# Performance work log

Hardware: AMD Instinct MI355X
Metric: run time of the kernel (lower is better)

Reference implementation:

```python
import jax, jax.numpy as jnp
import numpy as np

N = 50000      # nodes
E = 800000     # edges (before self-loops)
F_IN = 256     # input features
HID = 32       # per-head hidden channels, conv1
H1 = 4         # heads conv1 (concat)
H2 = 4         # heads conv2 (mean)
NCLS = 40      # output classes
NEG_SLOPE = 0.2
SM_EPS = 1e-16  # PyG softmax denominator eps
LN_EPS = 1e-5


def setup_inputs() -> dict:
    key = jax.random.key(0)
    ks = jax.random.split(key, 12)
    s1 = 1.0 / np.sqrt(F_IN)
    s2 = 1.0 / np.sqrt(H1 * HID)
    return {
        "x": jax.random.normal(ks[0], (N, F_IN), dtype=jnp.float32),
        "edge_index": jax.random.randint(ks[1], (2, E), 0, N, dtype=jnp.int32),
        "W1": jax.random.normal(ks[2], (F_IN, H1 * HID), dtype=jnp.float32) * s1,
        "att_src1": jax.random.normal(ks[3], (H1, HID), dtype=jnp.float32) * s1,
        "att_dst1": jax.random.normal(ks[4], (H1, HID), dtype=jnp.float32) * s1,
        "b1": jnp.zeros((H1 * HID,), jnp.float32),
        "W2": jax.random.normal(ks[5], (H1 * HID, H2 * NCLS), dtype=jnp.float32) * s2,
        "att_src2": jax.random.normal(ks[6], (H2, NCLS), dtype=jnp.float32) * s2,
        "att_dst2": jax.random.normal(ks[7], (H2, NCLS), dtype=jnp.float32) * s2,
        "b2": jnp.zeros((NCLS,), jnp.float32),
        "ln0_g": jnp.ones((H1 * HID,), jnp.float32),
        "ln0_b": jnp.zeros((H1 * HID,), jnp.float32),
        "ln1_g": jnp.ones((NCLS,), jnp.float32),
        "ln1_b": jnp.zeros((NCLS,), jnp.float32),
    }


def gat_conv(x, edge_index, W, a_src, a_dst, bias, heads, ch, concat):
    """PyG GATConv: self-loops, edge attention, per-dst segment softmax, scatter-sum."""
    n = x.shape[0]
    loops = jnp.arange(n, dtype=edge_index.dtype)
    src = jnp.concatenate([edge_index[0], loops])  # message source
    dst = jnp.concatenate([edge_index[1], loops])  # aggregation target
    h = (x @ W).reshape(n, heads, ch)              # [N,H,C]
    e_src = jnp.einsum('nhc,hc->nh', h, a_src)     # [N,H]
    e_dst = jnp.einsum('nhc,hc->nh', h, a_dst)
    e = jax.nn.leaky_relu(e_src[src] + e_dst[dst], NEG_SLOPE)  # [E',H]
    m = jax.ops.segment_max(e, dst, num_segments=n)            # stable softmax max
    p = jnp.exp(e - m[dst])
    denom = jax.ops.segment_sum(p, dst, num_segments=n)
    alpha = p / (denom[dst] + SM_EPS)                          # [E',H]
    out = jax.ops.segment_sum(h[src] * alpha[:, :, None], dst, num_segments=n)  # [N,H,C]
    out = out.reshape(n, heads * ch) if concat else out.mean(axis=1)
    return out + bias


def layer_norm(x, g, b):
    mu = x.mean(axis=-1, keepdims=True)
    var = jnp.mean((x - mu) ** 2, axis=-1, keepdims=True)
    return (x - mu) * jax.lax.rsqrt(var + LN_EPS) * g + b


def reference(x, edge_index, W1, att_src1, att_dst1, b1, W2, att_src2, att_dst2, b2,
              ln0_g, ln0_b, ln1_g, ln1_b):
    # eval mode: dropout = identity
    h = gat_conv(x, edge_index, W1, att_src1, att_dst1, b1, H1, HID, True)
    h = layer_norm(jax.nn.elu(h), ln0_g, ln0_b)
    h = gat_conv(h, edge_index, W2, att_src2, att_dst2, b2, H2, NCLS, False)
    h = layer_norm(h, ln1_g, ln1_b)
    return jax.nn.log_softmax(h, axis=1)
```

## Files before the change

### kernel.cpp

```cpp
#include <hip/hip_runtime.h>
#include <hip/hip_bf16.h>
#include <hip/hip_fp16.h>

#define NNODES 50000
#define NEDGES 800000
#define FIN    256
#define HEADS  4
#define C1     32
#define D1     128
#define C2     40
#define D2     160
#define CAP    64

#define RB1 144
#define RB2 88
#define ZB  ((NNODES + 255) / 256)
#define FB  (NEDGES / 256)
#define GB1 ((NNODES + 63) / 64)

typedef unsigned short u16;
typedef short v8s __attribute__((ext_vector_type(8)));
typedef float v4f __attribute__((ext_vector_type(4)));

__device__ __forceinline__ float bf2f(unsigned u) {
    union { unsigned u; float f; } x; x.u = u << 16; return x.f;
}
__device__ __forceinline__ u16 f2bf(float f) {
    unsigned u = __float_as_uint(f);
    return (u16)((u + 0x7fff + ((u >> 16) & 1)) >> 16);
}
__device__ __forceinline__ unsigned pk_bf16(float a, float b) {
    unsigned ua = (__float_as_uint(a) + 0x8000u) >> 16;
    unsigned ub = (__float_as_uint(b) + 0x8000u) & 0xffff0000u;
    return ub | ua;
}
__device__ __forceinline__ float wave_sum(float v) {
    #pragma unroll
    for (int m = 32; m > 0; m >>= 1) v += __shfl_xor(v, m, 64);
    return v;
}
__device__ __forceinline__ void wave_sum2(float& a, float& b) {
    #pragma unroll
    for (int m = 32; m > 0; m >>= 1) {
        a += __shfl_xor(a, m, 64);
        b += __shfl_xor(b, m, 64);
    }
}
__device__ __forceinline__ float leaky(float x) { return fmaxf(x, 0.2f * x); }

__device__ __forceinline__ void repack_body(const float* __restrict__ W,
                                            const float* __restrict__ as,
                                            const float* __restrict__ ad,
                                            u16* __restrict__ Wf,
                                            int K, int N, int C, int total, int idx) {
    if (idx >= total) return;
    int KS = K >> 5, NT = N >> 4;
    int j = idx & 7, lane = (idx >> 3) & 63;
    int rest = idx >> 9;
    int ks = rest % KS, nt = rest / KS;
    int k = ks * 32 + (lane >> 4) * 8 + j;
    int n16 = lane & 15;
    float val = 0.f;
    if (nt < NT) {
        val = W[(size_t)k * N + nt * 16 + n16];
    } else if (n16 < 8) {
        int h = n16 & 3;
        const float* av = (n16 < 4) ? as : ad;
        float s = 0.f;
        for (int c = 0; c < C; c++) s += W[(size_t)k * N + h * C + c] * av[h * C + c];
        val = s;
    }
    Wf[idx] = f2bf(val);
}

template <bool AF32, int KK, int NT>
__device__ __forceinline__ void gemm_body(const void* __restrict__ Aptr,
                                          const u16* __restrict__ Wf,
                                          u16* __restrict__ Out,
                                          float* __restrict__ ssrc,
                                          float* __restrict__ sdst, int M, int bid) {
    const int KS = KK / 32;
    const int NCOL = NT * 16;
    int wid = threadIdx.x >> 6, lane = threadIdx.x & 63;
    int r0 = bid * 64 + wid * 16;
    int m = lane & 15, quad = lane >> 4;
    int row = r0 + m;
    bool rowok = row < M;

    v8s a[KS];
    if (AF32) {
        const float* ap = (const float*)Aptr + (size_t)(rowok ? row : 0) * KK + quad * 8;
        #pragma unroll
        for (int ks = 0; ks < KS; ks++) {
            if (rowok) {
                float4 fa = *(const float4*)(ap + ks * 32);
                float4 fb = *(const float4*)(ap + ks * 32 + 4);
                union { unsigned u[4]; v8s v; } c;
                c.u[0] = pk_bf16(fa.x, fa.y); c.u[1] = pk_bf16(fa.z, fa.w);
                c.u[2] = pk_bf16(fb.x, fb.y); c.u[3] = pk_bf16(fb.z, fb.w);
                a[ks] = c.v;
            } else {
                a[ks] = (v8s){0,0,0,0,0,0,0,0};
            }
        }
    } else {
        const u16* ap = (const u16*)Aptr + (size_t)(rowok ? row : 0) * KK + quad * 8;
        #pragma unroll
        for (int ks = 0; ks < KS; ks++)
            a[ks] = rowok ? *(const v8s*)(ap + ks * 32) : (v8s){0,0,0,0,0,0,0,0};
    }

    const v8s* bp0 = (const v8s*)Wf + lane;
    #pragma unroll 2
    for (int nt = 0; nt < NT; nt++) {
        v4f acc = {0.f, 0.f, 0.f, 0.f};
        const v8s* bp = bp0 + nt * KS * 64;
        #pragma unroll
        for (int ks = 0; ks < KS; ks++)
            acc = __builtin_amdgcn_mfma_f32_16x16x32_bf16(a[ks], bp[ks * 64], acc, 0, 0, 0);
        int col = nt * 16 + m;
        #pragma unroll
        for (int reg = 0; reg < 4; reg++) {
            int r = r0 + quad * 4 + reg;
            if (r < M) Out[(size_t)r * NCOL + col] = f2bf(acc[reg]);
        }
    }
    {
        v4f acc = {0.f, 0.f, 0.f, 0.f};
        const v8s* bp = bp0 + NT * KS * 64;
        #pragma unroll
        for (int ks = 0; ks < KS; ks++)
            acc = __builtin_amdgcn_mfma_f32_16x16x32_bf16(a[ks], bp[ks * 64], acc, 0, 0, 0);
        if (m < 8) {
            float* tgt = (m < 4) ? ssrc : sdst;
            int h = m & 3;
            #pragma unroll
            for (int reg = 0; reg < 4; reg++) {
                int r = r0 + quad * 4 + reg;
                if (r < M) tgt[r * 4 + h] = acc[reg];
            }
        }
    }
}

__global__ __launch_bounds__(256) void repack_init(const float* __restrict__ W1,
                                                   const float* __restrict__ as1,
                                                   const float* __restrict__ ad1,
                                                   u16* __restrict__ Wf1,
                                                   const float* __restrict__ W2,
                                                   const float* __restrict__ as2,
                                                   const float* __restrict__ ad2,
                                                   u16* __restrict__ Wf2,
                                                   int* __restrict__ cursor,
                                                   u16* __restrict__ esrc) {
    int b = blockIdx.x;
    if (b < RB1) {
        repack_body(W1, as1, ad1, Wf1, FIN, D1, C1, 9 * 8 * 512, b * 256 + threadIdx.x);
    } else if (b < RB1 + RB2) {
        repack_body(W2, as2, ad2, Wf2, D1, D2, C2, 11 * 4 * 512, (b - RB1) * 256 + threadIdx.x);
    } else {
        int t = (b - RB1 - RB2) * 256 + threadIdx.x;
        if (t < NNODES) { cursor[t] = 1; esrc[t * CAP] = (u16)t; }
    }
}

__global__ __launch_bounds__(256) void gemm1_fill(const float* __restrict__ x,
                                                  const u16* __restrict__ Wf1,
                                                  u16* __restrict__ BH1,
                                                  float* __restrict__ ssrc,
                                                  float* __restrict__ sdst,
                                                  const int* __restrict__ ei,
                                                  int* __restrict__ cursor,
                                                  u16* __restrict__ esrc) {
    if (blockIdx.x < GB1) {
        gemm_body<true, FIN, 8>(x, Wf1, BH1, ssrc, sdst, NNODES, blockIdx.x);
    } else {
        int t = (blockIdx.x - GB1) * 256 + threadIdx.x;
        if (t >= NEDGES) return;
        int s = ei[t], d = ei[NEDGES + t];
        int pos = atomicAdd(&cursor[d], 1);
        esrc[d * CAP + pos] = (u16)s;
    }
}

#define PHASE_A32(SRC_ARR, P_ARR)                                                  \
    int nj = end - tb; if (nj > 32) nj = 32;                                       \
    bool on1 = jj < nj, on2 = jj + 16 < nj;                                        \
    int sE1 = on1 ? (int)esrc[tb + jj] : 0;                                        \
    int sE2 = on2 ? (int)esrc[tb + 16 + jj] : 0;                                   \
    if (hh == 0) { if (on1) SRC_ARR[wid][jj] = sE1;                                \
                   if (on2) SRC_ARR[wid][16 + jj] = sE2; }                         \
    float pa = on1 ? __expf(leaky(ssrc[sE1 * 4 + hh] + sdh)) : 0.f;                \
    float pb = on2 ? __expf(leaky(ssrc[sE2 * 4 + hh] + sdh)) : 0.f;                \
    float tsum = pa + pb;                                                          \
    tsum += __shfl_xor(tsum, 1, 64); tsum += __shfl_xor(tsum, 2, 64);              \
    tsum += __shfl_xor(tsum, 4, 64); tsum += __shfl_xor(tsum, 8, 64);              \
    den += tsum;                                                                   \
    if (on1) P_ARR[wid][hh][jj] = pa;                                              \
    if (on2) P_ARR[wid][hh][16 + jj] = pb;

__global__ __launch_bounds__(256) void gat_fused1(const int* __restrict__ cnt,
                                                  const u16* __restrict__ esrc,
                                                  const float* __restrict__ ssrc,
                                                  const float* __restrict__ sdst,
                                                  const u16* __restrict__ BH,
                                                  const float* __restrict__ b1,
                                                  const float* __restrict__ g,
                                                  const float* __restrict__ be,
                                                  const u16* __restrict__ Wf2,
                                                  u16* __restrict__ BH2,
                                                  float* __restrict__ ssrc2,
                                                  float* __restrict__ sdst2) {
    __shared__ int   s_src[4][32];
    __shared__ float s_p[4][4][32];
    __shared__ float s_den[4][4];
    int wid = threadIdx.x >> 6, lane = threadIdx.x & 63;
    int node = blockIdx.x * 4 + wid;
    int jj = lane & 15, hh = lane >> 4;
    int l8 = lane & 15, grp = lane >> 4;
    int head = l8 >> 2;
    float sdh = sdst[node * 4 + hh];
    int beg = node * CAP, end = beg + cnt[node];
    float den = 0.f;
    float acc[8];
    #pragma unroll
    for (int i = 0; i < 8; i++) acc[i] = 0.f;

    for (int tb = beg; tb < end; tb += 32) {
        PHASE_A32(s_src, s_p)
        #pragma unroll 8
        for (int j = grp; j < nj; j += 4) {
            int sj = s_src[wid][j];
            float al = s_p[wid][head][j];
            uint4 h = *(const uint4*)(BH + (size_t)sj * D1 + l8 * 8);
            acc[0] += al * bf2f(h.x & 0xffffu); acc[1] += al * bf2f(h.x >> 16);
            acc[2] += al * bf2f(h.y & 0xffffu); acc[3] += al * bf2f(h.y >> 16);
            acc[4] += al * bf2f(h.z & 0xffffu); acc[5] += al * bf2f(h.z >> 16);
            acc[6] += al * bf2f(h.w & 0xffffu); acc[7] += al * bf2f(h.w >> 16);
        }
    }
    if (jj == 0) s_den[wid][hh] = den;
    #pragma unroll
    for (int i = 0; i < 8; i++) {
        acc[i] += __shfl_xor(acc[i], 16, 64);
        acc[i] += __shfl_xor(acc[i], 32, 64);
    }
    float rden = 1.f / s_den[wid][head];
    float4 bA = *(const float4*)(b1 + l8 * 8), bB = *(const float4*)(b1 + l8 * 8 + 4);
    float v[8];
    v[0] = acc[0] * rden + bA.x; v[1] = acc[1] * rden + bA.y;
    v[2] = acc[2] * rden + bA.z; v[3] = acc[3] * rden + bA.w;
    v[4] = acc[4] * rden + bB.x; v[5] = acc[5] * rden + bB.y;
    v[6] = acc[6] * rden + bB.z; v[7] = acc[7] * rden + bB.w;
    float s8 = 0.f, q8 = 0.f;
    #pragma unroll
    for (int i = 0; i < 8; i++) {
        v[i] = v[i] > 0.f ? v[i] : __expf(v[i]) - 1.f;
        s8 += v[i]; q8 += v[i] * v[i];
    }
    wave_sum2(s8, q8);
    float mu = s8 * (1.f / 512.f);
    float var = q8 * (1.f / 512.f) - mu * mu;
    float rs = rsqrtf(var + 1e-5f);

    float4 gA = *(const float4*)(g + l8 * 8),  gB = *(const float4*)(g + l8 * 8 + 4);
    float4 eA = *(const float4*)(be + l8 * 8), eB = *(const float4*)(be + l8 * 8 + 4);
    float y[8];
    y[0] = (v[0] - mu) * rs * gA.x + eA.x; y[1] = (v[1] - mu) * rs * gA.y + eA.y;
    y[2] = (v[2] - mu) * rs * gA.z + eA.z; y[3] = (v[3] - mu) * rs * gA.w + eA.w;
    y[4] = (v[4] - mu) * rs * gB.x + eB.x; y[5] = (v[5] - mu) * rs * gB.y + eB.y;
    y[6] = (v[6] - mu) * rs * gB.z + eB.z; y[7] = (v[7] - mu) * rs * gB.w + eB.w;
    unsigned cpack[4];
    #pragma unroll
    for (int t = 0; t < 4; t++)
        cpack[t] = (unsigned)f2bf(y[2 * t]) | ((unsigned)f2bf(y[2 * t + 1]) << 16);

    union { unsigned u[4]; v8s v; } afr[4];
    #pragma unroll
    for (int ks = 0; ks < 4; ks++)
        #pragma unroll
        for (int t = 0; t < 4; t++)
            afr[ks].u[t] = __shfl(cpack[t], ks * 4 + grp, 64);

    const v8s* bp0 = (const v8s*)Wf2 + lane;
    #pragma unroll 2
    for (int nt = 0; nt < 10; nt++) {
        v4f a2 = {0.f, 0.f, 0.f, 0.f};
        const v8s* bp = bp0 + nt * 4 * 64;
        #pragma unroll
        for (int ks = 0; ks < 4; ks++)
            a2 = __builtin_amdgcn_mfma_f32_16x16x32_bf16(afr[ks].v, bp[ks * 64], a2, 0, 0, 0);
        if (grp == 0) BH2[(size_t)node * D2 + nt * 16 + l8] = f2bf(a2[0]);
    }
    {
        v4f a2 = {0.f, 0.f, 0.f, 0.f};
        const v8s* bp = bp0 + 10 * 4 * 64;
        #pragma unroll
        for (int ks = 0; ks < 4; ks++)
            a2 = __builtin_amdgcn_mfma_f32_16x16x32_bf16(afr[ks].v, bp[ks * 64], a2, 0, 0, 0);
        if (grp == 0 && l8 < 8) {
            float* tgt = (l8 < 4) ? ssrc2 : sdst2;
            tgt[node * 4 + (l8 & 3)] = a2[0];
        }
    }
}

__global__ __launch_bounds__(256) void gat_fused2(const int* __restrict__ cnt,
                                                  const u16* __restrict__ esrc,
                                                  const float* __restrict__ ssrc,
                                                  const float* __restrict__ sdst,
                                                  const u16* __restrict__ BH,
                                                  const float* __restrict__ b2,
                                                  const float* __restrict__ g,
                                                  const float* __restrict__ be,
                                                  float* __restrict__ out) {
    __shared__ int   s_src[4][32];
    __shared__ float s_p[4][4][32];
    __shared__ float s_den[4][4];
    __shared__ float scr3[4][3][160];
    int wid = threadIdx.x >> 6, lane = threadIdx.x & 63;
    int node = blockIdx.x * 4 + wid;
    int jj = lane & 15, hh = lane >> 4;
    int grp = lane / 20;
    int glane = lane - grp * 20;
    int head = glane / 5;
    float sdh = sdst[node * 4 + hh];
    int beg = node * CAP, end = beg + cnt[node];
    float den = 0.f;
    float acc[8];
    #pragma unroll
    for (int i = 0; i < 8; i++) acc[i] = 0.f;

    for (int tb = beg; tb < end; tb += 32) {
        PHASE_A32(s_src, s_p)
        if (grp < 3) {
            #pragma unroll 4
            for (int j = grp; j < nj; j += 3) {
                int sj = s_src[wid][j];
                float al = s_p[wid][head][j];
                uint4 h = *(const uint4*)(BH + (size_t)sj * D2 + glane * 8);
                acc[0] += al * bf2f(h.x & 0xffffu); acc[1] += al * bf2f(h.x >> 16);
                acc[2] += al * bf2f(h.y & 0xffffu); acc[3] += al * bf2f(h.y >> 16);
                acc[4] += al * bf2f(h.z & 0xffffu); acc[5] += al * bf2f(h.z >> 16);
                acc[6] += al * bf2f(h.w & 0xffffu); acc[7] += al * bf2f(h.w >> 16);
            }
        }
    }
    if (jj == 0) s_den[wid][hh] = den;
    if (grp < 3) {
        float rden = 1.f / s_den[wid][head];
        float4 oA = {acc[0] * rden, acc[1] * rden, acc[2] * rden, acc[3] * rden};
        float4 oB = {acc[4] * rden, acc[5] * rden, acc[6] * rden, acc[7] * rden};
        *(float4*)&scr3[wid][grp][glane * 8]     = oA;
        *(float4*)&scr3[wid][grp][glane * 8 + 4] = oB;
    }
    bool act = lane < 40;
    int c = act ? lane : 0;
    float o = 0.f;
    if (act) {
        float s = 0.f;
        #pragma unroll
        for (int k = 0; k < 4; k++)
            #pragma unroll
            for (int gg = 0; gg < 3; gg++) s += scr3[wid][gg][c + 40 * k];
        o = 0.25f * s + b2[c];
    }
    float so = act ? o : 0.f, qo = so * o;
    wave_sum2(so, qo);
    float mu = so * (1.f / 40.f);
    float var = qo * (1.f / 40.f) - mu * mu;
    float rs = rsqrtf(var + 1e-5f);
    float y = act ? (o - mu) * rs * g[c] + be[c] : 0.f;
    float ex = act ? __expf(y) : 0.f;
    float lse = __logf(wave_sum(ex));
    if (act) out[(size_t)node * 40 + c] = y - lse;
}

extern "C" void kernel_launch(void* const* d_in, const int* in_sizes, int n_in,
                              void* d_out, int out_size, void* d_ws, size_t ws_size,
                              hipStream_t stream) {
    const float* x   = (const float*)d_in[0];
    const int*   ei  = (const int*)d_in[1];
    const float* W1  = (const float*)d_in[2];
    const float* as1 = (const float*)d_in[3];
    const float* ad1 = (const float*)d_in[4];
    const float* b1  = (const float*)d_in[5];
    const float* W2  = (const float*)d_in[6];
    const float* as2 = (const float*)d_in[7];
    const float* ad2 = (const float*)d_in[8];
    const float* b2  = (const float*)d_in[9];
    const float* g0  = (const float*)d_in[10];
    const float* be0 = (const float*)d_in[11];
    const float* g1  = (const float*)d_in[12];
    const float* be1 = (const float*)d_in[13];

    float* ws = (float*)d_ws;
    u16*   BH1    = (u16*)ws;
    u16*   BH2    = (u16*)(ws + 3200000);
    float* ssrc   = ws + 7200000;
    float* sdst   = ws + 7400000;
    float* ssrc2  = ws + 7600000;
    float* sdst2  = ws + 7800000;
    u16*   esrc   = (u16*)(ws + 8000000);
    int*   cursor = (int*)(ws + 9600000);
    u16*   Wf1    = (u16*)(ws + 9650000);
    u16*   Wf2    = (u16*)(ws + 9668432);

    const int nb4 = NNODES / 4;

    repack_init<<<RB1 + RB2 + ZB, 256, 0, stream>>>(W1, as1, ad1, Wf1,
                                                    W2, as2, ad2, Wf2, cursor, esrc);
    gemm1_fill<<<GB1 + FB, 256, 0, stream>>>(x, Wf1, BH1, ssrc, sdst, ei, cursor, esrc);
    gat_fused1<<<nb4, 256, 0, stream>>>(cursor, esrc, ssrc, sdst, BH1, b1, g0, be0,
                                        Wf2, BH2, ssrc2, sdst2);
    gat_fused2<<<nb4, 256, 0, stream>>>(cursor, esrc, ssrc2, sdst2, BH2, b2, g1, be1,
                                        (float*)d_out);
}
```

Before: 308.2 us.

## Batch 16 nodes per block for layer-2 projection MFMA via shared memory

The first fused GAT kernel now uses 1024-thread blocks that each handle 16 nodes. It stages the normalized bf16 rows in shared memory so that 11 waves each compute one full 16x16 MFMA tile of the W2 projection. Before, each wave ran 11 MFMA tiles for a single node, with 15 of the 16 rows wasted. This cuts redundant matrix work and W2 fragment loads. The cost is a block-wide barrier and larger blocks, which may lower occupancy and tie the edge-loop latency of all 16 waves together; shared-memory padding is also added to the softmax arrays.

```diff
diff --git a/kernel.cpp b/kernel.cpp
--- a/kernel.cpp
+++ b/kernel.cpp
@@ -17,6 +17,7 @@
 #define ZB  ((NNODES + 255) / 256)
 #define FB  (NEDGES / 256)
 #define GB1 ((NNODES + 63) / 64)
+#define NB16 (NNODES / 16)
 
 typedef unsigned short u16;
 typedef short v8s __attribute__((ext_vector_type(8)));
@@ -199,23 +200,24 @@
     if (on1) P_ARR[wid][hh][jj] = pa;                                              \
     if (on2) P_ARR[wid][hh][16 + jj] = pb;
 
-__global__ __launch_bounds__(256) void gat_fused1(const int* __restrict__ cnt,
-                                                  const u16* __restrict__ esrc,
-                                                  const float* __restrict__ ssrc,
-                                                  const float* __restrict__ sdst,
-                                                  const u16* __restrict__ BH,
-                                                  const float* __restrict__ b1,
-                                                  const float* __restrict__ g,
-                                                  const float* __restrict__ be,
-                                                  const u16* __restrict__ Wf2,
-                                                  u16* __restrict__ BH2,
-                                                  float* __restrict__ ssrc2,
-                                                  float* __restrict__ sdst2) {
-    __shared__ int   s_src[4][32];
-    __shared__ float s_p[4][4][32];
-    __shared__ float s_den[4][4];
+__global__ __launch_bounds__(1024) void gat_fused1(const int* __restrict__ cnt,
+                                                   const u16* __restrict__ esrc,
+                                                   const float* __restrict__ ssrc,
+                                                   const float* __restrict__ sdst,
+                                                   const u16* __restrict__ BH,
+                                                   const float* __restrict__ b1,
+                                                   const float* __restrict__ g,
+                                                   const float* __restrict__ be,
+                                                   const u16* __restrict__ Wf2,
+                                                   u16* __restrict__ BH2,
+                                                   float* __restrict__ ssrc2,
+                                                   float* __restrict__ sdst2) {
+    __shared__ int   s_src[16][32];
+    __shared__ float s_p[16][4][33];
+    __shared__ float s_den[16][4];
+    __shared__ u16   s_af[4][4][17][8];
     int wid = threadIdx.x >> 6, lane = threadIdx.x & 63;
-    int node = blockIdx.x * 4 + wid;
+    int node = blockIdx.x * 16 + wid;
     int jj = lane & 15, hh = lane >> 4;
     int l8 = lane & 15, grp = lane >> 4;
     int head = l8 >> 2;
@@ -262,45 +264,47 @@
     float mu = s8 * (1.f / 512.f);
     float var = q8 * (1.f / 512.f) - mu * mu;
     float rs = rsqrtf(var + 1e-5f);
-
-    float4 gA = *(const float4*)(g + l8 * 8),  gB = *(const float4*)(g + l8 * 8 + 4);
-    float4 eA = *(const float4*)(be + l8 * 8), eB = *(const float4*)(be + l8 * 8 + 4);
-    float y[8];
-    y[0] = (v[0] - mu) * rs * gA.x + eA.x; y[1] = (v[1] - mu) * rs * gA.y + eA.y;
-    y[2] = (v[2] - mu) * rs * gA.z + eA.z; y[3] = (v[3] - mu) * rs * gA.w + eA.w;
-    y[4] = (v[4] - mu) * rs * gB.x + eB.x; y[5] = (v[5] - mu) * rs * gB.y + eB.y;
-    y[6] = (v[6] - mu) * rs * gB.z + eB.z; y[7] = (v[7] - mu) * rs * gB.w + eB.w;
-    unsigned cpack[4];
-    #pragma unroll
-    for (int t = 0; t < 4; t++)
-        cpack[t] = (unsigned)f2bf(y[2 * t]) | ((unsigned)f2bf(y[2 * t + 1]) << 16);
-
-    union { unsigned u[4]; v8s v; } afr[4];
-    #pragma unroll
-    for (int ks = 0; ks < 4; ks++)
-        #pragma unroll
-        for (int t = 0; t < 4; t++)
-            afr[ks].u[t] = __shfl(cpack[t], ks * 4 + grp, 64);
-
-    const v8s* bp0 = (const v8s*)Wf2 + lane;
-    #pragma unroll 2
-    for (int nt = 0; nt < 10; nt++) {
-        v4f a2 = {0.f, 0.f, 0.f, 0.f};
-        const v8s* bp = bp0 + nt * 4 * 64;
+    if (grp == 0) {
+        float4 gA = *(const float4*)(g + l8 * 8),  gB = *(const float4*)(g + l8 * 8 + 4);
+        float4 eA = *(const float4*)(be + l8 * 8), eB = *(const float4*)(be + l8 * 8 + 4);
+        unsigned c0 = (unsigned)f2bf((v[0] - mu) * rs * gA.x + eA.x)
+                    | ((unsigned)f2bf((v[1] - mu) * rs * gA.y + eA.y) << 16);
+        unsigned c1 = (unsigned)f2bf((v[2] - mu) * rs * gA.z + eA.z)
+                    | ((unsigned)f2bf((v[3] - mu) * rs * gA.w + eA.w) << 16);
+        unsigned c2 = (unsigned)f2bf((v[4] - mu) * rs * gB.x + eB.x)
+                    | ((unsigned)f2bf((v[5] - mu) * rs * gB.y + eB.y) << 16);
+        unsigned c3 = (unsigned)f2bf((v[6] - mu) * rs * gB.z + eB.z)
+                    | ((unsigned)f2bf((v[7] - mu) * rs * gB.w + eB.w) << 16);
+        *(uint4*)&s_af[l8 >> 2][l8 & 3][wid][0] = make_uint4(c0, c1, c2, c3);
+    }
+    __syncthreads();
+
+    if (wid < 11) {
+        int m2 = lane & 15, q2 = lane >> 4;
+        v8s a2[4];
         #pragma unroll
         for (int ks = 0; ks < 4; ks++)
-            a2 = __builtin_amdgcn_mfma_f32_16x16x32_bf16(afr[ks].v, bp[ks * 64], a2, 0, 0, 0);
-        if (grp == 0) BH2[(size_t)node * D2 + nt * 16 + l8] = f2bf(a2[0]);
-    }
-    {
-        v4f a2 = {0.f, 0.f, 0.f, 0.f};
-        const v8s* bp = bp0 + 10 * 4 * 64;
+            a2[ks] = *(const v8s*)&s_af[ks][q2][m2][0];
+        const v8s* bp = (const v8s*)Wf2 + wid * 4 * 64 + lane;
+        v4f acc2 = {0.f, 0.f, 0.f, 0.f};
         #pragma unroll
         for (int ks = 0; ks < 4; ks++)
-            a2 = __builtin_amdgcn_mfma_f32_16x16x32_bf16(afr[ks].v, bp[ks * 64], a2, 0, 0, 0);
-        if (grp == 0 && l8 < 8) {
-            float* tgt = (l8 < 4) ? ssrc2 : sdst2;
-            tgt[node * 4 + (l8 & 3)] = a2[0];
+            acc2 = __builtin_amdgcn_mfma_f32_16x16x32_bf16(a2[ks], bp[ks * 64], acc2, 0, 0, 0);
+        if (wid < 10) {
+            int col = wid * 16 + m2;
+            #pragma unroll
+            for (int reg = 0; reg < 4; reg++) {
+                int nd = blockIdx.x * 16 + q2 * 4 + reg;
+                BH2[(size_t)nd * D2 + col] = f2bf(acc2[reg]);
+            }
+        } else if (m2 < 8) {
+            float* tgt = (m2 < 4) ? ssrc2 : sdst2;
+            int h = m2 & 3;
+            #pragma unroll
+            for (int reg = 0; reg < 4; reg++) {
+                int nd = blockIdx.x * 16 + q2 * 4 + reg;
+                tgt[nd * 4 + h] = acc2[reg];
+            }
         }
     }
 }
@@ -315,7 +319,7 @@
                                                   const float* __restrict__ be,
                                                   float* __restrict__ out) {
     __shared__ int   s_src[4][32];
-    __shared__ float s_p[4][4][32];
+    __shared__ float s_p[4][4][33];
     __shared__ float s_den[4][4];
     __shared__ float scr3[4][3][160];
     int wid = threadIdx.x >> 6, lane = threadIdx.x & 63;
@@ -411,8 +415,8 @@
     repack_init<<<RB1 + RB2 + ZB, 256, 0, stream>>>(W1, as1, ad1, Wf1,
                                                     W2, as2, ad2, Wf2, cursor, esrc);
     gemm1_fill<<<GB1 + FB, 256, 0, stream>>>(x, Wf1, BH1, ssrc, sdst, ei, cursor, esrc);
-    gat_fused1<<<nb4, 256, 0, stream>>>(cursor, esrc, ssrc, sdst, BH1, b1, g0, be0,
-                                        Wf2, BH2, ssrc2, sdst2);
+    gat_fused1<<<NB16, 1024, 0, stream>>>(cursor, esrc, ssrc, sdst, BH1, b1, g0, be0,
+                                          Wf2, BH2, ssrc2, sdst2);
     gat_fused2<<<nb4, 256, 0, stream>>>(cursor, esrc, ssrc2, sdst2, BH2, b2, g1, be1,
                                         (float*)d_out);
 }
```

After: 260.2 us. 15.6% less time.
